# Kernel optimization log

Hardware: AMD Instinct MI355X
Metric: run time of the kernel (lower is better)

The kernel has to match this reference:

```python
import jax, jax.numpy as jnp
import numpy as np

EPS = 1e-5

def _bn(x, g, b, m, v):
    # inference-mode BatchNorm over channel axis 1
    shp = [1] * x.ndim
    shp[1] = x.shape[1]
    return (x - m.reshape(shp)) * (g.reshape(shp) / jnp.sqrt(v.reshape(shp) + EPS)) + b.reshape(shp)

def _forward(x, wdr, bdr, g1, be1, m1, v1, g2, be2, m2, v2, wrow, brow, wfc, bfc,
             wdrs, bdrs, g3, be3, m3, v3, g4, be4, m4, v4, wrows, brows, wfcs, bfcs):
    B, C, H, W = x.shape
    r = jax.nn.relu(x)

    # ---- channel attention (chan_att) ----
    y = jnp.einsum('bchw,oc->bohw', r, wdr) + bdr[None, :, None, None]   # 1x1 conv DR
    y = jax.nn.relu(_bn(y, g1, be1, m1, v1))
    Bc, D, _, _ = y.shape
    M = H * W
    yf = y.reshape(B, D, M)
    yc = yf - yf.mean(axis=2, keepdims=True)
    cov = jnp.einsum('bcm,bdm->bcd', yc, yc) / M                         # MPNCOV CovpoolLayer: x I_hat x^T, [B,D,D]
    cov = _bn(cov, g2, be2, m2, v2)                                      # row_bn (channel axis = D)
    # grouped conv: per-channel i, 4 filters over row i -> [B, D, 4]
    vch = jnp.einsum('bik,ijk->bij', cov, wrow).reshape(B, -1) + brow    # [B, 4D]
    catt = jax.nn.sigmoid(vch @ wfc.T + bfc)                             # fc_adapt_channels -> [B, C]
    catt = catt[:, :, None, None]

    # ---- spatial attention (pos_att) ----
    s = jnp.einsum('bchw,oc->bohw', r, wdrs) + bdrs[None, :, None, None]
    s = _bn(s, g3, be3, m3, v3)
    fh, fw = H // 8, W // 8
    sp = s.reshape(B, D, 8, fh, 8, fw).mean(axis=(3, 5))                 # adaptive avg pool -> 8x8
    M2 = 64
    sf = sp.reshape(B, D, M2)
    # cov_feature: x^T I_hat x with I_hat = (1/M2)(I_D - (1/M2) J_D)
    colsum = sf.sum(axis=1)                                              # [B, 64]
    covs = (jnp.einsum('bcm,bcn->bmn', sf, sf)
            - colsum[:, :, None] * colsum[:, None, :] / M2) / M2         # [B,64,64]
    covs = _bn(covs, g4, be4, m4, v4)
    vs = jnp.einsum('bik,ijk->bij', covs, wrows).reshape(B, -1) + brows  # [B,256]
    vs = jax.nn.relu(vs)
    patt = jax.nn.sigmoid(vs @ wfcs.T + bfcs)                            # [B,64]
    patt = patt.reshape(B, 1, 8, 8)
    patt = jnp.repeat(jnp.repeat(patt, fh, axis=2), fw, axis=3)          # adaptive unpool (exact replication)

    # attention == '+'
    return x * catt + jax.nn.relu(x * patt)

def setup_inputs() -> dict:
    key = jax.random.key(0)
    ks = jax.random.split(key, 32)
    B, C, H, W, D = 32, 512, 56, 56, 128
    n = lambda k, s, sc: jax.random.normal(k, s, dtype=jnp.float32) * sc
    u = lambda k, s: jax.random.uniform(k, s, dtype=jnp.float32)
    inp = {
        'x': n(ks[0], (B, C, H, W), 1.0),
        'wdr': n(ks[1], (D, C), 0.04), 'bdr': n(ks[2], (D,), 0.02),
        'g1': u(ks[3], (D,)) + 0.5, 'be1': n(ks[4], (D,), 0.1), 'm1': n(ks[5], (D,), 0.1), 'v1': u(ks[6], (D,)) * 0.5 + 0.5,
        'g2': u(ks[7], (D,)) + 0.5, 'be2': n(ks[8], (D,), 0.1), 'm2': n(ks[9], (D,), 0.1), 'v2': u(ks[10], (D,)) * 0.5 + 0.5,
        'wrow': n(ks[11], (D, 4, D), 0.08), 'brow': n(ks[12], (4 * D,), 0.02),
        'wfc': n(ks[13], (C, 4 * D), 0.04), 'bfc': n(ks[14], (C,), 0.02),
        'wdrs': n(ks[15], (D, C), 0.04), 'bdrs': n(ks[16], (D,), 0.02),
        'g3': u(ks[17], (D,)) + 0.5, 'be3': n(ks[18], (D,), 0.1), 'm3': n(ks[19], (D,), 0.1), 'v3': u(ks[20], (D,)) * 0.5 + 0.5,
        'g4': u(ks[21], (64,)) + 0.5, 'be4': n(ks[22], (64,), 0.1), 'm4': n(ks[23], (64,), 0.1), 'v4': u(ks[24], (64,)) * 0.5 + 0.5,
        'wrows': n(ks[25], (64, 4, 64), 0.1), 'brows': n(ks[26], (256,), 0.02),
        'wfcs': n(ks[27], (64, 256), 0.06), 'bfcs': n(ks[28], (64,), 0.02),
    }
    return inp

def reference(x, wdr, bdr, g1, be1, m1, v1, g2, be2, m2, v2, wrow, brow, wfc, bfc,
              wdrs, bdrs, g3, be3, m3, v3, g4, be4, m4, v4, wrows, brows, wfcs, bfcs):
    return _forward(x, wdr, bdr, g1, be1, m1, v1, g2, be2, m2, v2, wrow, brow, wfc, bfc,
                    wdrs, bdrs, g3, be3, m3, v3, g4, be4, m4, v4, wrows, brows, wfcs, bfcs)
```

## Files before the change

kernel.cpp:

```cpp
#include <hip/hip_runtime.h>
#include <hip/hip_bf16.h>

#define EPS 1e-5f

typedef short bf16x8 __attribute__((ext_vector_type(8)));
typedef float f32x4  __attribute__((ext_vector_type(4)));

union BF8 { ushort u[8]; bf16x8 v; };

__device__ __forceinline__ ushort f2bf(float f) {
  uint u = __float_as_uint(f);
  u += 0x7fffu + ((u >> 16) & 1u);
  return (ushort)(u >> 16);
}
__device__ __forceinline__ float bf2f(ushort u) {
  return __uint_as_float(((uint)u) << 16);
}
__device__ __forceinline__ f32x4 mfma16(bf16x8 a, bf16x8 b, f32x4 c) {
  return __builtin_amdgcn_mfma_f32_16x16x32_bf16(a, b, c, 0, 0, 0);
}

__device__ __forceinline__ void bar_lds() {
  asm volatile("s_waitcnt lgkmcnt(0)" ::: "memory");
  __builtin_amdgcn_s_barrier();
  __builtin_amdgcn_sched_barrier(0);
}

__global__ __launch_bounds__(256) void k_prep(
    const float* __restrict__ wdr, const float* __restrict__ wdrs,
    const float* __restrict__ bdr,
    const float* __restrict__ g1, const float* __restrict__ be1,
    const float* __restrict__ m1, const float* __restrict__ v1,
    const float* __restrict__ wfc,
    ushort* __restrict__ wdr_bf, ushort* __restrict__ wdrs_bf,
    float* __restrict__ sc1, float* __restrict__ sh1,
    float* __restrict__ wfcT, float4* __restrict__ zdst) {
  int i = blockIdx.x * 256 + threadIdx.x;
  zdst[i] = make_float4(0.f, 0.f, 0.f, 0.f);
  if (i < 65536) {
    wdr_bf[i]  = f2bf(wdr[i]);
    wdrs_bf[i] = f2bf(wdrs[i] * (1.0f / 49.0f));
  }
  if (i < 262144) {
    int c = i >> 9, p = i & 511;
    wfcT[p * 512 + c] = wfc[i];
  }
  if (i < 128) {
    float a = g1[i] / sqrtf(v1[i] + EPS);
    sc1[i] = a;
    sh1[i] = (bdr[i] - m1[i]) * a + be1[i];
  }
}

__global__ __launch_bounds__(256) void k_convy(
    const float* __restrict__ x, const ushort* __restrict__ wdr_bf,
    const float* __restrict__ sc1, const float* __restrict__ sh1,
    ushort* __restrict__ y_bf, float* __restrict__ rp) {
  __shared__ ushort xs[2][9216];
  __shared__ float pool[2][1024];
  __shared__ float sc_s[128], sh_s[128];

  const int t  = threadIdx.x;
  const int b  = blockIdx.y;
  const int n0 = blockIdx.x * 128;

  if (t < 128) { sc_s[t] = sc1[t]; sh_s[t] = sh1[t]; }
#pragma unroll
  for (int f = 0; f < 4; f++) { pool[0][t + f * 256] = 0.f; pool[1][t + f * 256] = 0.f; }

  const int cl = t & 7;
  const int nq = t >> 3;
  const int nl = nq * 4;
  const int ng = n0 + nl;
  const bool nv = ng < 3136;
  const int h   = ng / 56;
  const int w   = ng - h * 56;
  const int gh0 = (n0 / 56) / 7;
  const int lb0 = (h / 7 - gh0) * 8 + (w / 7);
  const int lb3 = (h / 7 - gh0) * 8 + ((w + 3) / 7);
  int split = 7 - (w % 7); if (split > 4) split = 4;
  const int ng8  = nq >> 1;
  const int nsub = (nq & 1) * 4;

  const int l  = t & 63;
  const int wv = t >> 6;
  const int wr = wv >> 1, wc = wv & 1;
  const int lm = l & 15,  lk = l >> 4;

  const float* xb = x + (size_t)(b * 512) * 3136 + ng;

  f32x4 acc[4][4];
#pragma unroll
  for (int a = 0; a < 4; a++)
#pragma unroll
    for (int c = 0; c < 4; c++) acc[a][c] = (f32x4){0.f, 0.f, 0.f, 0.f};

  const float4 z4 = make_float4(0.f, 0.f, 0.f, 0.f);
  float4 rA[8], rB[8];

#pragma unroll
  for (int r = 0; r < 8; r++) {
    rA[r] = z4;
    if (nv) rA[r] = *(const float4*)(xb + (size_t)(r * 8 + cl) * 3136);
  }

  __syncthreads();

  auto body = [&](int kc, float4 (&cur)[8], float4 (&nxt)[8]) {
    if (kc < 7) {
#pragma unroll
      for (int r = 0; r < 8; r++) {
        nxt[r] = z4;
        if (nv) nxt[r] = *(const float4*)(xb + (size_t)((kc + 1) * 64 + r * 8 + cl) * 3136);
      }
    }
    bf16x8 af_[2][4];
#pragma unroll
    for (int ki = 0; ki < 2; ki++)
#pragma unroll
      for (int mi = 0; mi < 4; mi++)
        af_[ki][mi] = *(const bf16x8*)(wdr_bf + (wr * 64 + mi * 16 + lm) * 512 + kc * 64 + ki * 32 + lk * 8);

    ushort* xsb = xs[kc & 1];
    float*  plb = pool[kc & 1];
#pragma unroll
    for (int r = 0; r < 8; r++) {
      int cc = r * 8 + cl;
      float e0 = fmaxf(cur[r].x, 0.f), e1 = fmaxf(cur[r].y, 0.f);
      float e2 = fmaxf(cur[r].z, 0.f), e3 = fmaxf(cur[r].w, 0.f);
      if (nv) {
        float s0 = e0, s1 = 0.f;
        if (split > 1) s0 += e1; else s1 += e1;
        if (split > 2) s0 += e2; else s1 += e2;
        if (split > 3) s0 += e3; else s1 += e3;
        atomicAdd(&plb[cc * 16 + lb0], s0);
        if (lb3 != lb0) atomicAdd(&plb[cc * 16 + lb3], s1);
      }
      int base = (cc >> 3) * 1152 + ng8 * 72 + nsub * 8 + (cc & 7);
      xsb[base]      = f2bf(e0);
      xsb[base + 8]  = f2bf(e1);
      xsb[base + 16] = f2bf(e2);
      xsb[base + 24] = f2bf(e3);
    }
    bar_lds();

#pragma unroll
    for (int ki = 0; ki < 2; ki++) {
      bf16x8 bfr[4];
#pragma unroll
      for (int ni = 0; ni < 4; ni++) {
        int n = wc * 64 + ni * 16 + lm;
        int a = (ki * 4 + lk) * 1152 + (n >> 3) * 72 + (n & 7) * 8;
        bfr[ni] = *(const bf16x8*)(xsb + a);
      }
#pragma unroll
      for (int mi = 0; mi < 4; mi++)
#pragma unroll
        for (int ni = 0; ni < 4; ni++)
          acc[mi][ni] = mfma16(af_[ki][mi], bfr[ni], acc[mi][ni]);
    }

#pragma unroll
    for (int f = 0; f < 4; f++) {
      int idx = t + f * 256;
      float pv = plb[idx];
      int cL = idx >> 4, lb = idx & 15;
      int gbin = gh0 * 8 + lb;
      if (pv != 0.f && gbin < 64)
        atomicAdd(&rp[((size_t)(b * 64 + gbin)) * 512 + kc * 64 + cL], pv);
      plb[idx] = 0.f;
    }
  };

  for (int kc2 = 0; kc2 < 8; kc2 += 2) {
    body(kc2,     rA, rB);
    body(kc2 + 1, rB, rA);
  }

#pragma unroll
  for (int mi = 0; mi < 4; mi++) {
#pragma unroll
    for (int ni = 0; ni < 4; ni++) {
      int n_g = n0 + wc * 64 + ni * 16 + lm;
      if (n_g >= 3136) continue;
#pragma unroll
      for (int r = 0; r < 4; r++) {
        int m = wr * 64 + mi * 16 + lk * 4 + r;
        float v = acc[mi][ni][r] * sc_s[m] + sh_s[m];
        v = fmaxf(v, 0.f);
        y_bf[((size_t)(b * 128 + m)) * 3136 + n_g] = f2bf(v);
      }
    }
  }
}

__global__ __launch_bounds__(256) void k_gram(
    const ushort* __restrict__ y_bf, float* __restrict__ G, float* __restrict__ S) {
  __shared__ ushort ys[2][128 * 40];
  const int t  = threadIdx.x;
  const int b  = blockIdx.y;
  const int k0 = blockIdx.x * 448;

  const int l  = t & 63, wv = t >> 6;
  const int wr = wv >> 1, wc = wv & 1;
  const int lm = l & 15,  lk = l >> 4;

  const int mA = t >> 2, k8 = t & 3;
  const ushort* yb = y_bf + ((size_t)(b * 128 + mA)) * 3136 + k0 + k8 * 8;
  const size_t rowoff = (size_t)64 * 3136;

  f32x4 acc[4][4];
#pragma unroll
  for (int a = 0; a < 4; a++)
#pragma unroll
    for (int c = 0; c < 4; c++) acc[a][c] = (f32x4){0.f, 0.f, 0.f, 0.f};
  float sA = 0.f, sB = 0.f;

  BF8 a0, a1, b0, b1;
  a0.v = *(const bf16x8*)(yb);
  a1.v = *(const bf16x8*)(yb + rowoff);

  auto gbody = [&](int kc, BF8& c0, BF8& c1, BF8& n0_, BF8& n1_) {
    if (kc < 13) {
      n0_.v = *(const bf16x8*)(yb + (kc + 1) * 32);
      n1_.v = *(const bf16x8*)(yb + rowoff + (kc + 1) * 32);
    }
#pragma unroll
    for (int j = 0; j < 8; j++) { sA += bf2f(c0.u[j]); sB += bf2f(c1.u[j]); }
    ushort* ysb = ys[kc & 1];
    *(bf16x8*)(ysb + mA * 40 + k8 * 8) = c0.v;
    *(bf16x8*)(ysb + (mA + 64) * 40 + k8 * 8) = c1.v;
    bar_lds();

    bf16x8 af[4], bfr[4];
#pragma unroll
    for (int mi = 0; mi < 4; mi++)
      af[mi] = *(const bf16x8*)(ysb + (wr * 64 + mi * 16 + lm) * 40 + lk * 8);
#pragma unroll
    for (int ni = 0; ni < 4; ni++)
      bfr[ni] = *(const bf16x8*)(ysb + (wc * 64 + ni * 16 + lm) * 40 + lk * 8);
#pragma unroll
    for (int mi = 0; mi < 4; mi++)
#pragma unroll
      for (int ni = 0; ni < 4; ni++)
        acc[mi][ni] = mfma16(af[mi], bfr[ni], acc[mi][ni]);
  };

  for (int kc2 = 0; kc2 < 14; kc2 += 2) {
    gbody(kc2,     a0, a1, b0, b1);
    gbody(kc2 + 1, b0, b1, a0, a1);
  }

#pragma unroll
  for (int mi = 0; mi < 4; mi++)
#pragma unroll
    for (int ni = 0; ni < 4; ni++)
#pragma unroll
      for (int r = 0; r < 4; r++) {
        int i = wr * 64 + mi * 16 + lk * 4 + r;
        int j = wc * 64 + ni * 16 + lm;
        atomicAdd(&G[((size_t)(b * 128 + i)) * 128 + j], acc[mi][ni][r]);
      }
  atomicAdd(&S[b * 128 + mA], sA);
  atomicAdd(&S[b * 128 + mA + 64], sB);
}

__global__ __launch_bounds__(256) void k_tail(
    const float* __restrict__ G, const float* __restrict__ S,
    const float* __restrict__ g2, const float* __restrict__ be2,
    const float* __restrict__ m2, const float* __restrict__ v2,
    const float* __restrict__ wrow, const float* __restrict__ brow,
    const float* __restrict__ wfcT, const float* __restrict__ bfc,
    const float* __restrict__ rp, const ushort* __restrict__ wdrs_bf,
    const float* __restrict__ bdrs,
    const float* __restrict__ g3, const float* __restrict__ be3,
    const float* __restrict__ m3, const float* __restrict__ v3,
    const float* __restrict__ g4, const float* __restrict__ be4,
    const float* __restrict__ m4, const float* __restrict__ v4,
    const float* __restrict__ wrows, const float* __restrict__ brows,
    const float* __restrict__ wfcs, const float* __restrict__ bfcs,
    float* __restrict__ catt, float* __restrict__ patt) {
  __shared__ float Ss[128];
  __shared__ float vch_s[512];
  __shared__ ushort sf_s[64 * 128];
  __shared__ float colsum_s[64];
  __shared__ float covbn_s[64 * 65];
  __shared__ float vs_s[256];
  const int t = threadIdx.x;
  const int b = blockIdx.x;

  const float invM = 1.0f / 3136.0f;
  if (t < 128) Ss[t] = S[b * 128 + t];
  __syncthreads();
#pragma unroll
  for (int rep = 0; rep < 2; rep++) {
    int p = t + rep * 256;
    int i = p >> 2, j = p & 3;
    float a2  = g2[i] / sqrtf(v2[i] + EPS);
    float mi2 = m2[i], bei = be2[i];
    float Si  = Ss[i] * invM;
    const float* Grow = G + ((size_t)(b * 128 + i)) * 128;
    const float* wr_  = wrow + (i * 4 + j) * 128;
    float a = 0.f;
    for (int k = 0; k < 128; k++) {
      float cov = (Grow[k] - Si * Ss[k]) * invM;
      a += ((cov - mi2) * a2 + bei) * wr_[k];
    }
    vch_s[p] = a + brow[p];
  }
  __syncthreads();
#pragma unroll
  for (int rep = 0; rep < 2; rep++) {
    int c = t + rep * 256;
    float z = bfc[c];
    for (int p = 0; p < 512; p++) z += vch_s[p] * wfcT[p * 512 + c];
    catt[b * 512 + c] = 1.f / (1.f + expf(-z));
  }

  {
    const int l = t & 63, wv = t >> 6;
    const int wm = wv >> 1, wn = wv & 1;
    const int lm = l & 15,  lk = l >> 4;
    f32x4 acc[4][2];
#pragma unroll
    for (int a = 0; a < 4; a++) { acc[a][0] = (f32x4){0.f,0.f,0.f,0.f}; acc[a][1] = (f32x4){0.f,0.f,0.f,0.f}; }

    for (int kk = 0; kk < 16; kk++) {
      bf16x8 af[4], bfr[2];
#pragma unroll
      for (int mi = 0; mi < 4; mi++) {
        int m = wm * 64 + mi * 16 + lm;
        af[mi] = *(const bf16x8*)(wdrs_bf + m * 512 + kk * 32 + lk * 8);
      }
#pragma unroll
      for (int ni = 0; ni < 2; ni++) {
        int g = wn * 32 + ni * 16 + lm;
        const float* pb = rp + ((size_t)(b * 64 + g)) * 512 + kk * 32 + lk * 8;
        float4 fa = *(const float4*)pb;
        float4 fb = *(const float4*)(pb + 4);
        BF8 bb;
        bb.u[0] = f2bf(fa.x); bb.u[1] = f2bf(fa.y); bb.u[2] = f2bf(fa.z); bb.u[3] = f2bf(fa.w);
        bb.u[4] = f2bf(fb.x); bb.u[5] = f2bf(fb.y); bb.u[6] = f2bf(fb.z); bb.u[7] = f2bf(fb.w);
        bfr[ni] = bb.v;
      }
#pragma unroll
      for (int mi = 0; mi < 4; mi++)
#pragma unroll
        for (int ni = 0; ni < 2; ni++)
          acc[mi][ni] = mfma16(af[mi], bfr[ni], acc[mi][ni]);
    }
#pragma unroll
    for (int mi = 0; mi < 4; mi++)
#pragma unroll
      for (int ni = 0; ni < 2; ni++) {
        int g = wn * 32 + ni * 16 + lm;
#pragma unroll
        for (int r = 0; r < 4; r++) {
          int d = wm * 64 + mi * 16 + lk * 4 + r;
          float a3 = g3[d] / sqrtf(v3[d] + EPS);
          float sf = (acc[mi][ni][r] + bdrs[d] - m3[d]) * a3 + be3[d];
          sf_s[g * 128 + d] = f2bf(sf);
        }
      }
  }
  __syncthreads();

  if (t < 64) {
    float cs = 0.f;
    const ushort* row = sf_s + t * 128;
    for (int dq = 0; dq < 16; dq++) {
      BF8 v; v.v = *(const bf16x8*)(row + dq * 8);
#pragma unroll
      for (int j = 0; j < 8; j++) cs += bf2f(v.u[j]);
    }
    colsum_s[t] = cs;
  }
  __syncthreads();

  {
    const int l = t & 63, wv = t >> 6;
    const int wr = wv >> 1, wc = wv & 1;
    const int lm = l & 15,  lk = l >> 4;
    f32x4 acc[2][2];
    acc[0][0] = (f32x4){0.f,0.f,0.f,0.f}; acc[0][1] = (f32x4){0.f,0.f,0.f,0.f};
    acc[1][0] = (f32x4){0.f,0.f,0.f,0.f}; acc[1][1] = (f32x4){0.f,0.f,0.f,0.f};
    for (int kk = 0; kk < 4; kk++) {
      bf16x8 af[2], bfr[2];
#pragma unroll
      for (int mi = 0; mi < 2; mi++)
        af[mi] = *(const bf16x8*)(sf_s + (wr * 32 + mi * 16 + lm) * 128 + kk * 32 + lk * 8);
#pragma unroll
      for (int ni = 0; ni < 2; ni++)
        bfr[ni] = *(const bf16x8*)(sf_s + (wc * 32 + ni * 16 + lm) * 128 + kk * 32 + lk * 8);
#pragma unroll
      for (int mi = 0; mi < 2; mi++)
#pragma unroll
        for (int ni = 0; ni < 2; ni++)
          acc[mi][ni] = mfma16(af[mi], bfr[ni], acc[mi][ni]);
    }
    const float inv64 = 1.0f / 64.0f;
#pragma unroll
    for (int mi = 0; mi < 2; mi++)
#pragma unroll
      for (int ni = 0; ni < 2; ni++) {
        int j = wc * 32 + ni * 16 + lm;
#pragma unroll
        for (int r = 0; r < 4; r++) {
          int i = wr * 32 + mi * 16 + lk * 4 + r;
          float cv = (acc[mi][ni][r] - colsum_s[i] * colsum_s[j] * inv64) * inv64;
          float a4 = g4[i] / sqrtf(v4[i] + EPS);
          covbn_s[i * 65 + j] = (cv - m4[i]) * a4 + be4[i];
        }
      }
  }
  __syncthreads();
  {
    int m = t >> 2, j = t & 3;
    float a = brows[t];
    const float* wr_ = wrows + (m * 4 + j) * 64;
    for (int k = 0; k < 64; k++) a += covbn_s[m * 65 + k] * wr_[k];
    vs_s[t] = fmaxf(a, 0.f);
  }
  __syncthreads();
  if (t < 64) {
    float z = bfcs[t];
    const float* wf = wfcs + t * 256;
    for (int p = 0; p < 256; p++) z += vs_s[p] * wf[p];
    patt[b * 64 + t] = 1.f / (1.f + expf(-z));
  }
}

__global__ __launch_bounds__(256) void k_final(
    const float* __restrict__ x, const float* __restrict__ catt,
    const float* __restrict__ patt, float* __restrict__ out) {
  int gi = blockIdx.x * 256 + threadIdx.x;
  int bc = gi / 784;
  int q  = gi - bc * 784;
  int n  = q * 4;
  int b  = bc >> 9;
  float ca = catt[bc];
  int h = n / 56;
  int w = n - h * 56;
  const float* pp = patt + b * 64 + (h / 7) * 8;
  float p0 = pp[w / 7], p1 = pp[(w + 1) / 7], p2 = pp[(w + 2) / 7], p3 = pp[(w + 3) / 7];
  float4 xv = *(const float4*)(x + (size_t)gi * 4);
  float4 o;
  o.x = xv.x * ca + fmaxf(xv.x * p0, 0.f);
  o.y = xv.y * ca + fmaxf(xv.y * p1, 0.f);
  o.z = xv.z * ca + fmaxf(xv.z * p2, 0.f);
  o.w = xv.w * ca + fmaxf(xv.w * p3, 0.f);
  *(float4*)(out + (size_t)gi * 4) = o;
}

extern "C" void kernel_launch(void* const* d_in, const int* in_sizes, int n_in,
                              void* d_out, int out_size, void* d_ws, size_t ws_size,
                              hipStream_t stream) {
  const float* x     = (const float*)d_in[0];
  const float* wdr   = (const float*)d_in[1];
  const float* bdr   = (const float*)d_in[2];
  const float* g1    = (const float*)d_in[3];
  const float* be1   = (const float*)d_in[4];
  const float* m1    = (const float*)d_in[5];
  const float* v1    = (const float*)d_in[6];
  const float* g2    = (const float*)d_in[7];
  const float* be2   = (const float*)d_in[8];
  const float* m2    = (const float*)d_in[9];
  const float* v2    = (const float*)d_in[10];
  const float* wrow  = (const float*)d_in[11];
  const float* brow  = (const float*)d_in[12];
  const float* wfc   = (const float*)d_in[13];
  const float* bfc   = (const float*)d_in[14];
  const float* wdrs  = (const float*)d_in[15];
  const float* bdrs  = (const float*)d_in[16];
  const float* g3    = (const float*)d_in[17];
  const float* be3   = (const float*)d_in[18];
  const float* m3    = (const float*)d_in[19];
  const float* v3    = (const float*)d_in[20];
  const float* g4    = (const float*)d_in[21];
  const float* be4   = (const float*)d_in[22];
  const float* m4    = (const float*)d_in[23];
  const float* v4    = (const float*)d_in[24];
  const float* wrows = (const float*)d_in[25];
  const float* brows = (const float*)d_in[26];
  const float* wfcs  = (const float*)d_in[27];
  const float* bfcs  = (const float*)d_in[28];

  char* ob = (char*)d_out;
  ushort* y_bf    = (ushort*)(ob + 0x0000000);
  ushort* wdr_bf  = (ushort*)(ob + 0x2000000);
  ushort* wdrs_bf = (ushort*)(ob + 0x2020000);
  float*  sc1     = (float*) (ob + 0x2040000);
  float*  sh1     = (float*) (ob + 0x2040200);
  float*  wfcT    = (float*) (ob + 0x2050000);
  float*  rp      = (float*) (ob + 0x2150000);
  float*  G       = (float*) (ob + 0x2550000);
  float*  S       = (float*) (ob + 0x2750000);
  ushort* sfT     = (ushort*)(ob + 0x2760000);
  (void)sfT;

  char* ws = (char*)d_ws;
  float* catt = (float*)(ws + 0x00000);
  float* patt = (float*)(ws + 0x10000);

  k_prep<<<1540, 256, 0, stream>>>(wdr, wdrs, bdr, g1, be1, m1, v1, wfc,
                                   wdr_bf, wdrs_bf, sc1, sh1, wfcT,
                                   (float4*)(ob + 0x2150000));
  k_convy<<<dim3(25, 32), 256, 0, stream>>>(x, wdr_bf, sc1, sh1, y_bf, rp);
  k_gram<<<dim3(7, 32), 256, 0, stream>>>(y_bf, G, S);
  k_tail<<<32, 256, 0, stream>>>(G, S, g2, be2, m2, v2, wrow, brow, wfcT, bfc,
                                 rp, wdrs_bf, bdrs, g3, be3, m3, v3,
                                 g4, be4, m4, v4, wrows, brows, wfcs, bfcs,
                                 catt, patt);
  k_final<<<50176, 256, 0, stream>>>(x, catt, patt, (float*)d_out);
}
```

Baseline: 704.2 us.

## Fuse Gram matrix computation into conv kernel via LDS-resident y tile

The separate k_gram kernel is removed. k_convy now writes its 128x128 post-BN/ReLU tile into shared memory and computes the partial Gram matrix and row sums directly from LDS, accumulating them into G and S with atomics. This drops the bf16 y round-trip through global memory and one kernel launch, at the cost of more atomics (25 tiles per batch instead of 7) and a longer conv kernel. The global prefetch of the next x chunk and the weight loads are also moved after the LDS barrier, with a sched_barrier between them.

```diff
diff --git a/kernel.cpp b/kernel.cpp
--- a/kernel.cpp
+++ b/kernel.cpp
@@ -55,7 +55,7 @@
 __global__ __launch_bounds__(256) void k_convy(
     const float* __restrict__ x, const ushort* __restrict__ wdr_bf,
     const float* __restrict__ sc1, const float* __restrict__ sh1,
-    ushort* __restrict__ y_bf, float* __restrict__ rp) {
+    float* __restrict__ rp, float* __restrict__ G, float* __restrict__ S) {
   __shared__ ushort xs[2][9216];
   __shared__ float pool[2][1024];
   __shared__ float sc_s[128], sh_s[128];
@@ -107,20 +107,6 @@
   __syncthreads();
 
   auto body = [&](int kc, float4 (&cur)[8], float4 (&nxt)[8]) {
-    if (kc < 7) {
-#pragma unroll
-      for (int r = 0; r < 8; r++) {
-        nxt[r] = z4;
-        if (nv) nxt[r] = *(const float4*)(xb + (size_t)((kc + 1) * 64 + r * 8 + cl) * 3136);
-      }
-    }
-    bf16x8 af_[2][4];
-#pragma unroll
-    for (int ki = 0; ki < 2; ki++)
-#pragma unroll
-      for (int mi = 0; mi < 4; mi++)
-        af_[ki][mi] = *(const bf16x8*)(wdr_bf + (wr * 64 + mi * 16 + lm) * 512 + kc * 64 + ki * 32 + lk * 8);
-
     ushort* xsb = xs[kc & 1];
     float*  plb = pool[kc & 1];
 #pragma unroll
@@ -144,6 +130,21 @@
     }
     bar_lds();
 
+    bf16x8 af_[2][4];
+#pragma unroll
+    for (int ki = 0; ki < 2; ki++)
+#pragma unroll
+      for (int mi = 0; mi < 4; mi++)
+        af_[ki][mi] = *(const bf16x8*)(wdr_bf + (wr * 64 + mi * 16 + lm) * 512 + kc * 64 + ki * 32 + lk * 8);
+    __builtin_amdgcn_sched_barrier(0);
+    if (kc < 7) {
+#pragma unroll
+      for (int r = 0; r < 8; r++) {
+        nxt[r] = z4;
+        if (nv) nxt[r] = *(const float4*)(xb + (size_t)((kc + 1) * 64 + r * 8 + cl) * 3136);
+      }
+    }
+
 #pragma unroll
     for (int ki = 0; ki < 2; ki++) {
       bf16x8 bfr[4];
@@ -177,80 +178,58 @@
     body(kc2 + 1, rB, rA);
   }
 
+  __syncthreads();
+  ushort* yt = &xs[0][0];
+  const int YS = 136;
+
 #pragma unroll
   for (int mi = 0; mi < 4; mi++) {
 #pragma unroll
     for (int ni = 0; ni < 4; ni++) {
-      int n_g = n0 + wc * 64 + ni * 16 + lm;
-      if (n_g >= 3136) continue;
+      int col = wc * 64 + ni * 16 + lm;
+      int n_g = n0 + col;
+      bool cv_ = n_g < 3136;
 #pragma unroll
       for (int r = 0; r < 4; r++) {
         int m = wr * 64 + mi * 16 + lk * 4 + r;
-        float v = acc[mi][ni][r] * sc_s[m] + sh_s[m];
-        v = fmaxf(v, 0.f);
-        y_bf[((size_t)(b * 128 + m)) * 3136 + n_g] = f2bf(v);
-      }
-    }
-  }
-}
-
-__global__ __launch_bounds__(256) void k_gram(
-    const ushort* __restrict__ y_bf, float* __restrict__ G, float* __restrict__ S) {
-  __shared__ ushort ys[2][128 * 40];
-  const int t  = threadIdx.x;
-  const int b  = blockIdx.y;
-  const int k0 = blockIdx.x * 448;
-
-  const int l  = t & 63, wv = t >> 6;
-  const int wr = wv >> 1, wc = wv & 1;
-  const int lm = l & 15,  lk = l >> 4;
-
-  const int mA = t >> 2, k8 = t & 3;
-  const ushort* yb = y_bf + ((size_t)(b * 128 + mA)) * 3136 + k0 + k8 * 8;
-  const size_t rowoff = (size_t)64 * 3136;
-
-  f32x4 acc[4][4];
+        float v = cv_ ? fmaxf(acc[mi][ni][r] * sc_s[m] + sh_s[m], 0.f) : 0.f;
+        yt[m * YS + col] = f2bf(v);
+      }
+    }
+  }
+  __syncthreads();
+
+  if (t < 128) {
+    float cs = 0.f;
+#pragma unroll
+    for (int dq = 0; dq < 16; dq++) {
+      BF8 v8; v8.v = *(const bf16x8*)(yt + t * YS + dq * 8);
+#pragma unroll
+      for (int j = 0; j < 8; j++) cs += bf2f(v8.u[j]);
+    }
+    atomicAdd(&S[b * 128 + t], cs);
+  }
+
+  f32x4 g[4][4];
 #pragma unroll
   for (int a = 0; a < 4; a++)
 #pragma unroll
-    for (int c = 0; c < 4; c++) acc[a][c] = (f32x4){0.f, 0.f, 0.f, 0.f};
-  float sA = 0.f, sB = 0.f;
-
-  BF8 a0, a1, b0, b1;
-  a0.v = *(const bf16x8*)(yb);
-  a1.v = *(const bf16x8*)(yb + rowoff);
-
-  auto gbody = [&](int kc, BF8& c0, BF8& c1, BF8& n0_, BF8& n1_) {
-    if (kc < 13) {
-      n0_.v = *(const bf16x8*)(yb + (kc + 1) * 32);
-      n1_.v = *(const bf16x8*)(yb + rowoff + (kc + 1) * 32);
-    }
-#pragma unroll
-    for (int j = 0; j < 8; j++) { sA += bf2f(c0.u[j]); sB += bf2f(c1.u[j]); }
-    ushort* ysb = ys[kc & 1];
-    *(bf16x8*)(ysb + mA * 40 + k8 * 8) = c0.v;
-    *(bf16x8*)(ysb + (mA + 64) * 40 + k8 * 8) = c1.v;
-    bar_lds();
-
-    bf16x8 af[4], bfr[4];
+    for (int c = 0; c < 4; c++) g[a][c] = (f32x4){0.f, 0.f, 0.f, 0.f};
+#pragma unroll
+  for (int kk = 0; kk < 4; kk++) {
+    bf16x8 ag[4], bg[4];
 #pragma unroll
     for (int mi = 0; mi < 4; mi++)
-      af[mi] = *(const bf16x8*)(ysb + (wr * 64 + mi * 16 + lm) * 40 + lk * 8);
+      ag[mi] = *(const bf16x8*)(yt + (wr * 64 + mi * 16 + lm) * YS + kk * 32 + lk * 8);
 #pragma unroll
     for (int ni = 0; ni < 4; ni++)
-      bfr[ni] = *(const bf16x8*)(ysb + (wc * 64 + ni * 16 + lm) * 40 + lk * 8);
+      bg[ni] = *(const bf16x8*)(yt + (wc * 64 + ni * 16 + lm) * YS + kk * 32 + lk * 8);
 #pragma unroll
     for (int mi = 0; mi < 4; mi++)
 #pragma unroll
       for (int ni = 0; ni < 4; ni++)
-        acc[mi][ni] = mfma16(af[mi], bfr[ni], acc[mi][ni]);
-  };
-
-  for (int kc2 = 0; kc2 < 14; kc2 += 2) {
-    gbody(kc2,     a0, a1, b0, b1);
-    gbody(kc2 + 1, b0, b1, a0, a1);
-  }
-
+        g[mi][ni] = mfma16(ag[mi], bg[ni], g[mi][ni]);
+  }
 #pragma unroll
   for (int mi = 0; mi < 4; mi++)
 #pragma unroll
@@ -259,10 +238,8 @@
       for (int r = 0; r < 4; r++) {
         int i = wr * 64 + mi * 16 + lk * 4 + r;
         int j = wc * 64 + ni * 16 + lm;
-        atomicAdd(&G[((size_t)(b * 128 + i)) * 128 + j], acc[mi][ni][r]);
-      }
-  atomicAdd(&S[b * 128 + mA], sA);
-  atomicAdd(&S[b * 128 + mA + 64], sB);
+        atomicAdd(&G[((size_t)(b * 128 + i)) * 128 + j], g[mi][ni][r]);
+      }
 }
 
 __global__ __launch_bounds__(256) void k_tail(
@@ -486,7 +463,6 @@
   const float* bfcs  = (const float*)d_in[28];
 
   char* ob = (char*)d_out;
-  ushort* y_bf    = (ushort*)(ob + 0x0000000);
   ushort* wdr_bf  = (ushort*)(ob + 0x2000000);
   ushort* wdrs_bf = (ushort*)(ob + 0x2020000);
   float*  sc1     = (float*) (ob + 0x2040000);
@@ -495,8 +471,6 @@
   float*  rp      = (float*) (ob + 0x2150000);
   float*  G       = (float*) (ob + 0x2550000);
   float*  S       = (float*) (ob + 0x2750000);
-  ushort* sfT     = (ushort*)(ob + 0x2760000);
-  (void)sfT;
 
   char* ws = (char*)d_ws;
   float* catt = (float*)(ws + 0x00000);
@@ -505,8 +479,7 @@
   k_prep<<<1540, 256, 0, stream>>>(wdr, wdrs, bdr, g1, be1, m1, v1, wfc,
                                    wdr_bf, wdrs_bf, sc1, sh1, wfcT,
                                    (float4*)(ob + 0x2150000));
-  k_convy<<<dim3(25, 32), 256, 0, stream>>>(x, wdr_bf, sc1, sh1, y_bf, rp);
-  k_gram<<<dim3(7, 32), 256, 0, stream>>>(y_bf, G, S);
+  k_convy<<<dim3(25, 32), 256, 0, stream>>>(x, wdr_bf, sc1, sh1, rp, G, S);
   k_tail<<<32, 256, 0, stream>>>(G, S, g2, be2, m2, v2, wrow, brow, wfcT, bfc,
                                  rp, wdrs_bf, bdrs, g3, be3, m3, v3,
                                  g4, be4, m4, v4, wrows, brows, wfcs, bfcs,
```

After: 721.1 us. 1.02x slower.
